# Kernel tuning notes

Hardware: AMD Instinct MI355X
Metric: run time of the kernel (lower is better)

## Reference

```python
import jax, jax.numpy as jnp
import numpy as np

WIN = 10  # self.len in the torch module


def setup_inputs() -> dict:
    key = jax.random.key(0)
    # [batch, seq_length, agent_num, vel]
    inputs = jax.random.normal(key, (8, 512, 96, 2), dtype=jnp.float32)
    return {"inputs": inputs}


def reference(inputs):
    # Faithful vectorization of the triple loop:
    #                    / sqrt(sum xc_i^2 * sum xc_j^2)
    # (the (seq_length*vel - 1) normalizers in cov/std cancel exactly)
    B, S, A, V = inputs.shape
    xc = inputs - inputs.mean(axis=1, keepdims=True)  # center over time
    # per-timestep pairwise Gram over the tiny vel dim: [B, S, A, A]
    g = jnp.einsum('bsiv,bsjv->bsij', xc, xc)
    # sliding-window sums via cumulative-sum trick
    C = jnp.cumsum(g, axis=1)                         # [B, S, A, A]
    head = C[:, :S - 1]                               # window end at step s (s=1..S-1)
    tail = jnp.concatenate(
        [jnp.zeros((B, WIN, A, A), C.dtype), C[:, :S - 1 - WIN]], axis=1)
    W = head - tail                                   # windowed Gram [B, S-1, A, A]
    d = jnp.diagonal(W, axis1=2, axis2=3)             # windowed energy [B, S-1, A]
    corr = W / jnp.sqrt(d[..., :, None] * d[..., None, :])
    # torch code never writes the diagonal -> stays zero
    mask = 1.0 - jnp.eye(A, dtype=corr.dtype)
    return corr * mask
```

## Files before the change

### kernel.cpp

```cpp
#include <hip/hip_runtime.h>

constexpr int WIN = 10;
constexpr int Bn  = 8;
constexpr int Sn  = 512;
constexpr int An  = 96;
constexpr int Tn  = Sn - 1;
constexpr int AV  = An * 2;

constexpr int SCHUNK = 32;
constexpr int NCH    = Sn / SCHUNK;
constexpr int CH     = 16;
constexpr int CHUNKS_PER_B = (Tn + CH - 1) / CH;
constexpr int MAXROWS = CH + WIN - 1;
constexpr int ISPLIT  = 4;
constexpr int ROWS    = An / ISPLIT;
constexpr int NTHR    = 192;
constexpr int TXN     = 24;
constexpr int TYN     = NTHR / TXN;
constexpr int RPT     = ROWS / TYN;

__global__ __launch_bounds__(192)
void partial_kernel(const float* __restrict__ in, float* __restrict__ partial) {
    const int blk = blockIdx.x;
    const int b   = blk / NCH;
    const int c   = blk - b * NCH;
    const int av  = threadIdx.x;
    const float* p = in + ((size_t)(b * Sn + c * SCHUNK)) * AV + av;
    float acc = 0.f;
    #pragma unroll
    for (int s = 0; s < SCHUNK; ++s) acc += p[(size_t)s * AV];
    partial[(size_t)blk * AV + av] = acc;
}

__global__ __launch_bounds__(192)
void corr_kernel(const float* __restrict__ in, const float* __restrict__ partial,
                 float* __restrict__ out) {
    __shared__ __align__(16) float xw[MAXROWS * AV];
    __shared__ __align__(16) float smu[AV];

    const int bid     = blockIdx.x;
    const int b       = bid / (CHUNKS_PER_B * ISPLIT);
    const int rem     = bid - b * (CHUNKS_PER_B * ISPLIT);
    const int chunk   = rem >> 2;
    const int quarter = rem & 3;
    const int i0      = quarter * ROWS;

    const int t0 = chunk * CH;
    const int t1 = min(t0 + CH - 1, Tn - 1);
    int sbase = t0 - (WIN - 1); if (sbase < 0) sbase = 0;
    const int nrows = t1 - sbase + 1;

    const int tid = threadIdx.x;

    {
        const float* pp = partial + (size_t)b * NCH * AV + tid;
        float acc = 0.f;
        #pragma unroll
        for (int c = 0; c < NCH; ++c) acc += pp[(size_t)c * AV];
        smu[tid] = acc * (1.0f / Sn);
    }
    __syncthreads();

    {
        const float4* src = reinterpret_cast<const float4*>(
            in + ((size_t)(b * Sn + sbase)) * AV);
        const float4* mb4 = reinterpret_cast<const float4*>(smu);
        float4* dst = reinterpret_cast<float4*>(xw);
        const int tot4 = nrows * (AV / 4);
        for (int idx = tid; idx < tot4; idx += NTHR) {
            int av4 = idx % (AV / 4);
            float4 v = src[idx], m = mb4[av4];
            v.x -= m.x; v.y -= m.y; v.z -= m.z; v.w -= m.w;
            dst[idx] = v;
        }
    }
    __syncthreads();

    const int tx = tid % TXN;
    const int ty = tid / TXN;

    float acc[RPT][4];
    float di[RPT], dj[4];
    #pragma unroll
    for (int r = 0; r < RPT; ++r) {
        di[r] = 0.f;
        #pragma unroll
        for (int c = 0; c < 4; ++c) acc[r][c] = 0.f;
    }
    #pragma unroll
    for (int c = 0; c < 4; ++c) dj[c] = 0.f;

#define ACCUM(ls, OP)                                                        \
    {                                                                        \
        const float* xs = &xw[(ls) * AV];                                    \
        float4 xj0 = *reinterpret_cast<const float4*>(&xs[8 * tx]);          \
        float4 xj1 = *reinterpret_cast<const float4*>(&xs[8 * tx + 4]);      \
        dj[0] OP (xj0.x * xj0.x + xj0.y * xj0.y);                            \
        dj[1] OP (xj0.z * xj0.z + xj0.w * xj0.w);                            \
        dj[2] OP (xj1.x * xj1.x + xj1.y * xj1.y);                            \
        dj[3] OP (xj1.z * xj1.z + xj1.w * xj1.w);                            \
        _Pragma("unroll")                                                    \
        for (int r = 0; r < RPT; ++r) {                                      \
            float2 xi = *reinterpret_cast<const float2*>(                    \
                &xs[(i0 + ty + 8 * r) * 2]);                                 \
            di[r] OP (xi.x * xi.x + xi.y * xi.y);                            \
            acc[r][0] OP (xi.x * xj0.x + xi.y * xj0.y);                      \
            acc[r][1] OP (xi.x * xj0.z + xi.y * xj0.w);                      \
            acc[r][2] OP (xi.x * xj1.x + xi.y * xj1.y);                      \
            acc[r][3] OP (xi.x * xj1.z + xi.y * xj1.w);                      \
        }                                                                    \
    }

    auto emit = [&](int t) {
        float rsj[4];
        #pragma unroll
        for (int c = 0; c < 4; ++c) rsj[c] = rsqrtf(dj[c]);
        float* ob = out + (size_t)(b * Tn + t) * (An * An);
        #pragma unroll
        for (int r = 0; r < RPT; ++r) {
            int i = i0 + ty + 8 * r;
            float ri = rsqrtf(di[r]);
            float4 v;
            v.x = (i == 4 * tx + 0) ? 0.f : acc[r][0] * ri * rsj[0];
            v.y = (i == 4 * tx + 1) ? 0.f : acc[r][1] * ri * rsj[1];
            v.z = (i == 4 * tx + 2) ? 0.f : acc[r][2] * ri * rsj[2];
            v.w = (i == 4 * tx + 3) ? 0.f : acc[r][3] * ri * rsj[3];
            *reinterpret_cast<float4*>(&ob[(size_t)i * An + 4 * tx]) = v;
        }
    };

    for (int s = sbase; s <= t0; ++s) ACCUM(s - sbase, +=);
    emit(t0);

    for (int t = t0 + 1; t <= t1; ++t) {
        ACCUM(t - sbase, +=);
        if (t >= WIN) ACCUM(t - WIN - sbase, -=);
        emit(t);
    }
#undef ACCUM
}

extern "C" void kernel_launch(void* const* d_in, const int* in_sizes, int n_in,
                              void* d_out, int out_size, void* d_ws, size_t ws_size,
                              hipStream_t stream) {
    const float* in = (const float*)d_in[0];
    float* out = (float*)d_out;
    float* partial = (float*)d_ws;

    partial_kernel<<<Bn * NCH, 192, 0, stream>>>(in, partial);
    corr_kernel<<<Bn * CHUNKS_PER_B * ISPLIT, NTHR, 0, stream>>>(in, partial, out);
}
```

Baseline: 40.58 us.

## Fuse mean reduction into corr kernel with atomic producers and grid flag

Removes the separate partial-sum kernel. The first 64 blocks of the correlation kernel now compute per-batch time sums, combine them with float atomics into a workspace, and bump a global counter. Every block copies its raw input window into shared memory first, then spins on the counter before reading the means and centering in place. This saves a kernel launch and overlaps the mean computation with the input load, but it adds a memset and relies on all producer blocks being co-resident, which risks a deadlock. Float atomics also make the means order-nondeterministic.

```diff
diff --git a/kernel.cpp b/kernel.cpp
--- a/kernel.cpp
+++ b/kernel.cpp
@@ -7,8 +7,6 @@
 constexpr int Tn  = Sn - 1;
 constexpr int AV  = An * 2;
 
-constexpr int SCHUNK = 32;
-constexpr int NCH    = Sn / SCHUNK;
 constexpr int CH     = 16;
 constexpr int CHUNKS_PER_B = (Tn + CH - 1) / CH;
 constexpr int MAXROWS = CH + WIN - 1;
@@ -19,24 +17,19 @@
 constexpr int TYN     = NTHR / TXN;
 constexpr int RPT     = ROWS / TYN;
 
-__global__ __launch_bounds__(192)
-void partial_kernel(const float* __restrict__ in, float* __restrict__ partial) {
-    const int blk = blockIdx.x;
-    const int b   = blk / NCH;
-    const int c   = blk - b * NCH;
-    const int av  = threadIdx.x;
-    const float* p = in + ((size_t)(b * Sn + c * SCHUNK)) * AV + av;
-    float acc = 0.f;
-    #pragma unroll
-    for (int s = 0; s < SCHUNK; ++s) acc += p[(size_t)s * AV];
-    partial[(size_t)blk * AV + av] = acc;
-}
+constexpr int NPROD   = 64;
+constexpr int PPB     = NPROD / Bn;
+constexpr int PROWS   = Sn / PPB;
 
-__global__ __launch_bounds__(192)
-void corr_kernel(const float* __restrict__ in, const float* __restrict__ partial,
-                 float* __restrict__ out) {
+
+__global__ __launch_bounds__(NTHR)
+void corr_fused(const float* __restrict__ in, float* __restrict__ ws,
+                float* __restrict__ out) {
     __shared__ __align__(16) float xw[MAXROWS * AV];
     __shared__ __align__(16) float smu[AV];
+
+    float* meanbuf = ws;
+    int*   flag    = reinterpret_cast<int*>(ws + Bn * AV);
 
     const int bid     = blockIdx.x;
     const int b       = bid / (CHUNKS_PER_B * ISPLIT);
@@ -52,24 +45,66 @@
 
     const int tid = threadIdx.x;
 
+    if (bid < NPROD) {
+        const int pb = bid >> 3;
+        const int pp = bid & 7;
+        const float4* src = reinterpret_cast<const float4*>(in)
+                          + ((size_t)pb * Sn + pp * PROWS) * (AV / 4);
+        const int q  = tid % (AV / 4);
+        const int rg = tid / (AV / 4);
+        float4 s = make_float4(0.f, 0.f, 0.f, 0.f);
+        #pragma unroll
+        for (int r = 0; r < PROWS / 4; ++r) {
+            float4 v = src[(size_t)(rg + 4 * r) * (AV / 4) + q];
+            s.x += v.x; s.y += v.y; s.z += v.z; s.w += v.w;
+        }
+        float4* red = reinterpret_cast<float4*>(xw);
+        red[rg * (AV / 4) + q] = s;
+        __syncthreads();
+        if (rg == 0) {
+            float4 a = red[q], b1 = red[48 + q], c1 = red[96 + q], d1 = red[144 + q];
+            a.x += b1.x + c1.x + d1.x;
+            a.y += b1.y + c1.y + d1.y;
+            a.z += b1.z + c1.z + d1.z;
+            a.w += b1.w + c1.w + d1.w;
+            atomicAdd(&meanbuf[pb * AV + 4 * q + 0], a.x);
+            atomicAdd(&meanbuf[pb * AV + 4 * q + 1], a.y);
+            atomicAdd(&meanbuf[pb * AV + 4 * q + 2], a.z);
+            atomicAdd(&meanbuf[pb * AV + 4 * q + 3], a.w);
+        }
+        __threadfence();
+        __syncthreads();
+        if (tid == 0)
+            __hip_atomic_fetch_add(flag, 1, __ATOMIC_RELEASE,
+                                   __HIP_MEMORY_SCOPE_AGENT);
+        __syncthreads();
+    }
+
     {
-        const float* pp = partial + (size_t)b * NCH * AV + tid;
-        float acc = 0.f;
-        #pragma unroll
-        for (int c = 0; c < NCH; ++c) acc += pp[(size_t)c * AV];
-        smu[tid] = acc * (1.0f / Sn);
+        const float4* src4 = reinterpret_cast<const float4*>(in)
+                           + ((size_t)(b * Sn + sbase)) * (AV / 4);
+        float4* dst = reinterpret_cast<float4*>(xw);
+        const int tot4 = nrows * (AV / 4);
+        for (int idx = tid; idx < tot4; idx += NTHR) dst[idx] = src4[idx];
     }
     __syncthreads();
 
+    if (tid == 0) {
+        while (__hip_atomic_load(flag, __ATOMIC_ACQUIRE,
+                                 __HIP_MEMORY_SCOPE_AGENT) < NPROD)
+            __builtin_amdgcn_s_sleep(8);
+    }
+    __syncthreads();
+    __threadfence();
+
+    smu[tid] = meanbuf[b * AV + tid] * (1.0f / Sn);
+    __syncthreads();
     {
-        const float4* src = reinterpret_cast<const float4*>(
-            in + ((size_t)(b * Sn + sbase)) * AV);
-        const float4* mb4 = reinterpret_cast<const float4*>(smu);
         float4* dst = reinterpret_cast<float4*>(xw);
+        const float4* smu4 = reinterpret_cast<const float4*>(smu);
         const int tot4 = nrows * (AV / 4);
         for (int idx = tid; idx < tot4; idx += NTHR) {
-            int av4 = idx % (AV / 4);
-            float4 v = src[idx], m = mb4[av4];
+            float4 v = dst[idx], m = smu4[idx % (AV / 4)];
             v.x -= m.x; v.y -= m.y; v.z -= m.z; v.w -= m.w;
             dst[idx] = v;
         }
@@ -131,7 +166,6 @@
 
     for (int s = sbase; s <= t0; ++s) ACCUM(s - sbase, +=);
     emit(t0);
-
     for (int t = t0 + 1; t <= t1; ++t) {
         ACCUM(t - sbase, +=);
         if (t >= WIN) ACCUM(t - WIN - sbase, -=);
@@ -145,8 +179,8 @@
                               hipStream_t stream) {
     const float* in = (const float*)d_in[0];
     float* out = (float*)d_out;
-    float* partial = (float*)d_ws;
+    float* ws  = (float*)d_ws;
 
-    partial_kernel<<<Bn * NCH, 192, 0, stream>>>(in, partial);
-    corr_kernel<<<Bn * CHUNKS_PER_B * ISPLIT, NTHR, 0, stream>>>(in, partial, out);
+    hipMemsetAsync(d_ws, 0, (Bn * AV + 1) * sizeof(float), stream);
+    corr_fused<<<Bn * CHUNKS_PER_B * ISPLIT, NTHR, 0, stream>>>(in, ws, out);
 }
```

Result: slower. 120.0 us (+195.6%).

## Pad shared-memory rows and precompute windowed rsqrt norms in a pre-pass

Applied to the files above, without the earlier changes.

The centered window rows in shared memory now use a padded layout (36 floats per 32) so the float4 and float2 reads in the accumulation loop avoid LDS bank conflicts. The per-agent windowed energies and their rsqrt are computed once per timestep by 96 threads into a shared table, replacing the redundant di/dj accumulation and per-element rsqrt in every thread. This cuts FMAs and transcendentals in the inner loop. The cost is an extra serial pre-pass, an added barrier and more shared memory per block.

```diff
diff --git a/kernel.cpp b/kernel.cpp
--- a/kernel.cpp
+++ b/kernel.cpp
@@ -19,6 +19,9 @@
 constexpr int TYN     = NTHR / TXN;
 constexpr int RPT     = ROWS / TYN;
 
+constexpr int SWR = 216;
+__device__ __forceinline__ int swoff(int f) { return (f >> 5) * 36 + (f & 31); }
+
 __global__ __launch_bounds__(192)
 void partial_kernel(const float* __restrict__ in, float* __restrict__ partial) {
     const int blk = blockIdx.x;
@@ -35,7 +38,8 @@
 __global__ __launch_bounds__(192)
 void corr_kernel(const float* __restrict__ in, const float* __restrict__ partial,
                  float* __restrict__ out) {
-    __shared__ __align__(16) float xw[MAXROWS * AV];
+    __shared__ __align__(16) float xw[MAXROWS * SWR];
+    __shared__ __align__(16) float rs[CH][An];
     __shared__ __align__(16) float smu[AV];
 
     const int bid     = blockIdx.x;
@@ -68,42 +72,59 @@
         float4* dst = reinterpret_cast<float4*>(xw);
         const int tot4 = nrows * (AV / 4);
         for (int idx = tid; idx < tot4; idx += NTHR) {
-            int av4 = idx % (AV / 4);
-            float4 v = src[idx], m = mb4[av4];
+            int row = idx / (AV / 4);
+            int q   = idx - row * (AV / 4);
+            float4 v = src[idx], m = mb4[q];
             v.x -= m.x; v.y -= m.y; v.z -= m.z; v.w -= m.w;
-            dst[idx] = v;
+            dst[row * (SWR / 4) + (q >> 3) * 9 + (q & 7)] = v;
+        }
+    }
+    __syncthreads();
+
+    if (tid < An) {
+        const int off = swoff(2 * tid);
+        float d = 0.f;
+        for (int s = sbase; s <= t0; ++s) {
+            float x0 = xw[(s - sbase) * SWR + off];
+            float x1 = xw[(s - sbase) * SWR + off + 1];
+            d += x0 * x0 + x1 * x1;
+        }
+        rs[0][tid] = rsqrtf(d);
+        for (int t = t0 + 1; t <= t1; ++t) {
+            float x0 = xw[(t - sbase) * SWR + off];
+            float x1 = xw[(t - sbase) * SWR + off + 1];
+            d += x0 * x0 + x1 * x1;
+            if (t >= WIN) {
+                float y0 = xw[(t - WIN - sbase) * SWR + off];
+                float y1 = xw[(t - WIN - sbase) * SWR + off + 1];
+                d -= y0 * y0 + y1 * y1;
+            }
+            rs[t - t0][tid] = rsqrtf(d);
         }
     }
     __syncthreads();
 
     const int tx = tid % TXN;
     const int ty = tid / TXN;
+    const int oj = swoff(8 * tx);
+    int oi[RPT];
+    #pragma unroll
+    for (int r = 0; r < RPT; ++r) oi[r] = swoff(2 * (i0 + ty + 8 * r));
 
     float acc[RPT][4];
-    float di[RPT], dj[4];
     #pragma unroll
-    for (int r = 0; r < RPT; ++r) {
-        di[r] = 0.f;
+    for (int r = 0; r < RPT; ++r)
         #pragma unroll
         for (int c = 0; c < 4; ++c) acc[r][c] = 0.f;
-    }
-    #pragma unroll
-    for (int c = 0; c < 4; ++c) dj[c] = 0.f;
 
 #define ACCUM(ls, OP)                                                        \
     {                                                                        \
-        const float* xs = &xw[(ls) * AV];                                    \
-        float4 xj0 = *reinterpret_cast<const float4*>(&xs[8 * tx]);          \
-        float4 xj1 = *reinterpret_cast<const float4*>(&xs[8 * tx + 4]);      \
-        dj[0] OP (xj0.x * xj0.x + xj0.y * xj0.y);                            \
-        dj[1] OP (xj0.z * xj0.z + xj0.w * xj0.w);                            \
-        dj[2] OP (xj1.x * xj1.x + xj1.y * xj1.y);                            \
-        dj[3] OP (xj1.z * xj1.z + xj1.w * xj1.w);                            \
+        const float* xs = &xw[(ls) * SWR];                                   \
+        float4 xj0 = *reinterpret_cast<const float4*>(&xs[oj]);              \
+        float4 xj1 = *reinterpret_cast<const float4*>(&xs[oj + 4]);          \
         _Pragma("unroll")                                                    \
         for (int r = 0; r < RPT; ++r) {                                      \
-            float2 xi = *reinterpret_cast<const float2*>(                    \
-                &xs[(i0 + ty + 8 * r) * 2]);                                 \
-            di[r] OP (xi.x * xi.x + xi.y * xi.y);                            \
+            float2 xi = *reinterpret_cast<const float2*>(&xs[oi[r]]);        \
             acc[r][0] OP (xi.x * xj0.x + xi.y * xj0.y);                      \
             acc[r][1] OP (xi.x * xj0.z + xi.y * xj0.w);                      \
             acc[r][2] OP (xi.x * xj1.x + xi.y * xj1.y);                      \
@@ -112,19 +133,18 @@
     }
 
     auto emit = [&](int t) {
-        float rsj[4];
-        #pragma unroll
-        for (int c = 0; c < 4; ++c) rsj[c] = rsqrtf(dj[c]);
+        const int tt = t - t0;
+        float4 rsj = *reinterpret_cast<const float4*>(&rs[tt][4 * tx]);
         float* ob = out + (size_t)(b * Tn + t) * (An * An);
         #pragma unroll
         for (int r = 0; r < RPT; ++r) {
             int i = i0 + ty + 8 * r;
-            float ri = rsqrtf(di[r]);
+            float ri = rs[tt][i];
             float4 v;
-            v.x = (i == 4 * tx + 0) ? 0.f : acc[r][0] * ri * rsj[0];
-            v.y = (i == 4 * tx + 1) ? 0.f : acc[r][1] * ri * rsj[1];
-            v.z = (i == 4 * tx + 2) ? 0.f : acc[r][2] * ri * rsj[2];
-            v.w = (i == 4 * tx + 3) ? 0.f : acc[r][3] * ri * rsj[3];
+            v.x = (i == 4 * tx + 0) ? 0.f : acc[r][0] * ri * rsj.x;
+            v.y = (i == 4 * tx + 1) ? 0.f : acc[r][1] * ri * rsj.y;
+            v.z = (i == 4 * tx + 2) ? 0.f : acc[r][2] * ri * rsj.z;
+            v.w = (i == 4 * tx + 3) ? 0.f : acc[r][3] * ri * rsj.w;
             *reinterpret_cast<float4*>(&ob[(size_t)i * An + 4 * tx]) = v;
         }
     };
```

New measurement: 42.45 us. +4.6%, slower.
